# Optimization experiments

Hardware: AMD Instinct MI355X
Metric: run time of the kernel (lower is better)

Reference implementation:

```python
import jax, jax.numpy as jnp
import numpy as np

TOP_K = 4
EPS = 1e-6


def setup_inputs() -> dict:
    key = jax.random.key(0)
    k1, k2, k3 = jax.random.split(key, 3)
    B, Q, N, H, W = 4, 200, 32, 256, 256
    pred_masks = jax.random.normal(k1, (B, Q, H, W), dtype=jnp.float32)
    pred_logits = jax.random.normal(k2, (B, Q, 2), dtype=jnp.float32)
    gt_masks = (jax.random.uniform(k3, (B, N, H, W)) < 0.3).astype(jnp.float32)
    return {"pred_masks": pred_masks, "pred_logits": pred_logits, "gt_masks": gt_masks}


def _combined_scores(pred_masks, pred_logits, gt_masks):
    """IoU * class-score, shape [B, Q, N]."""
    pm = jax.nn.sigmoid(pred_masks)                    # [B,Q,H,W]
    cls = jax.nn.softmax(pred_logits, axis=-1)[..., 1]  # [B,Q]
    B, Q = pm.shape[:2]
    N = gt_masks.shape[1]
    pmf = pm.reshape(B, Q, -1)                         # [B,Q,D]
    tmf = gt_masks.reshape(B, N, -1)                   # [B,N,D]
    inter = jnp.einsum('bqd,bnd->bqn', pmf, tmf)
    union = pmf.sum(-1)[:, :, None] + tmf.sum(-1)[:, None, :] - inter
    iou = inter / (union + EPS)
    return iou * cls[:, :, None]


def _greedy_assign(combined):
    """Greedy per-GT top-k with dedup. combined: [Q,N] -> sel indices [N,k], -1 = dropped."""
    Q = combined.shape[0]
    k = min(TOP_K, Q)

    def step(assigned, col):
        _, idx = jax.lax.top_k(col, k)          # [k] query indices for this GT
        taken = assigned[idx]                   # already assigned -> drop
        sel = jnp.where(taken, -1, idx)
        assigned = assigned.at[idx].set(True)
        return assigned, sel

    _, sels = jax.lax.scan(step, jnp.zeros(Q, dtype=bool), combined.T)
    return sels  # [N, k]


def reference(pred_masks, pred_logits, gt_masks):
    combined = _combined_scores(pred_masks, pred_logits, gt_masks)  # [B,Q,N]
    sels = jax.vmap(_greedy_assign)(combined)                       # [B,N,k]
    B, N, k = sels.shape
    src_idx = sels
    tgt_idx = jnp.broadcast_to(jnp.arange(N, dtype=jnp.int32)[None, :, None], sels.shape)
    valid = sels >= 0
    tgt_idx = jnp.where(valid, tgt_idx, -1)
    return src_idx, tgt_idx, valid
```

## Files before the change

kernel.cpp:

```cpp
#include <hip/hip_runtime.h>
#include <math.h>
#include <stdint.h>

#define BB    4
#define QQ    200
#define NGT   32
#define DD    65536
#define TOPK  4
#define EPSF  1e-6f
#define QP    208

#define QT3   7
#define KS    32
#define KC    (DD / KS)
#define BK    128
#define NCH   (KC / BK)
#define NSTEP (BK / 16)
#define BKP   (BK + 8)

typedef float  f32x4  __attribute__((ext_vector_type(4)));
typedef float  f32x16 __attribute__((ext_vector_type(16)));
typedef __bf16 bf16x8 __attribute__((ext_vector_type(8)));

__global__ __launch_bounds__(256) void k_pack(const float* __restrict__ gt,
                                              uint32_t* __restrict__ packed,
                                              float* __restrict__ zero_base) {
    int zidx = blockIdx.x * 256 + threadIdx.x;
    if (zidx < BB * NGT * QP + BB * QP) zero_base[zidx] = 0.0f;

    int blk = blockIdx.x;
    int b = blk >> 6;
    int d0 = ((blk & 63) * 256 + threadIdx.x) * 4;
    uint32_t px = 0, py = 0, pz = 0, pw = 0;
    const float* gb = gt + (size_t)b * NGT * DD + d0;
#pragma unroll
    for (int n = 0; n < NGT; ++n) {
        float4 g = *(const float4*)(gb + (size_t)n * DD);
        px |= (g.x > 0.5f ? 1u : 0u) << n;
        py |= (g.y > 0.5f ? 1u : 0u) << n;
        pz |= (g.z > 0.5f ? 1u : 0u) << n;
        pw |= (g.w > 0.5f ? 1u : 0u) << n;
    }
    *(uint4*)(packed + (size_t)b * DD + d0) = make_uint4(px, py, pz, pw);
}

__global__ __launch_bounds__(256) void k_tsum(const uint32_t* __restrict__ packed,
                                              float* __restrict__ tsum,
                                              const float* __restrict__ logits,
                                              float* __restrict__ cls) {
    if (blockIdx.x < 4) {
        int i = blockIdx.x * 256 + threadIdx.x;
        if (i < BB * QQ) {
            float l0 = logits[2 * i], l1 = logits[2 * i + 1];
            cls[i] = 1.0f / (1.0f + expf(l0 - l1));
        }
    }
    int b = blockIdx.x >> 5;
    int n = blockIdx.x & 31;
    const uint4* pp = (const uint4*)(packed + (size_t)b * DD);
    int cnt = 0;
    for (int i = threadIdx.x; i < DD / 4; i += 256) {
        uint4 w = pp[i];
        cnt += (int)((w.x >> n) & 1u) + (int)((w.y >> n) & 1u) +
               (int)((w.z >> n) & 1u) + (int)((w.w >> n) & 1u);
    }
#pragma unroll
    for (int off = 32; off; off >>= 1) cnt += __shfl_xor(cnt, off);
    __shared__ int red[4];
    if ((threadIdx.x & 63) == 0) red[threadIdx.x >> 6] = cnt;
    __syncthreads();
    if (threadIdx.x == 0)
        tsum[blockIdx.x] = (float)(red[0] + red[1] + red[2] + red[3]);
}

__global__ __launch_bounds__(256, 3) void k_mfma(const float* __restrict__ pm,
                                                 const uint32_t* __restrict__ packed,
                                                 float* __restrict__ inter,
                                                 float* __restrict__ psum) {
    int blk = blockIdx.x;
    int b   = blk / (QT3 * KS);
    int rem = blk % (QT3 * KS);
    int qt  = rem / KS;
    int ks  = rem % KS;
    int tid = threadIdx.x, lane = tid & 63, wave = tid >> 6;

    __shared__ __bf16 aA[3][32][BKP];
    __shared__ uint32_t bfrag[NSTEP * 256];

    int q_local = tid >> 3;
    int dseg    = (tid & 7) * 16;
    int q_glob  = qt * 32 + q_local;
    int q_eff   = q_glob < QQ ? q_glob : QQ - 1;
    const float*    pmrow = pm + (size_t)(b * QQ + q_eff) * DD + ks * KC;
    const uint32_t* pk    = packed + (size_t)b * DD + ks * KC;

    int l0  = (tid * 2) & 63;
    int bst = tid >> 5;
    int bko = bst * 16 + ((l0 >> 5) << 3);
    int sh0 = 31 - (l0 & 31);
    int sh1 = 31 - ((l0 + 1) & 31);

    int m    = lane & 31;
    int half = lane >> 5;

    f32x16 ch_, cm_, cl_;
#pragma unroll
    for (int r = 0; r < 16; ++r) { ch_[r] = 0.f; cm_[r] = 0.f; cl_[r] = 0.f; }
    float ps = 0.f;

    for (int ch = 0; ch < NCH; ++ch) {
        const float* src = pmrow + ch * BK + dseg;
        float4 f0 = *(const float4*)(src);
        float4 f1 = *(const float4*)(src + 4);
        float4 f2 = *(const float4*)(src + 8);
        float4 f3 = *(const float4*)(src + 12);
        float xv[16] = {f0.x, f0.y, f0.z, f0.w, f1.x, f1.y, f1.z, f1.w,
                        f2.x, f2.y, f2.z, f2.w, f3.x, f3.y, f3.z, f3.w};
        uint32_t hd[8], md[8], ld[8];
#pragma unroll
        for (int p = 0; p < 8; ++p) {
            uint32_t uh[2], um[2], ul[2];
#pragma unroll
            for (int e = 0; e < 2; ++e) {
                float x = xv[2 * p + e];
                float s = __builtin_amdgcn_rcpf(1.0f + __expf(-x));
                ps += s;
                uint32_t u0 = __float_as_uint(s);
                float hi = __uint_as_float(u0 & 0xFFFF0000u);
                float r1 = s - hi;
                uint32_t u1 = __float_as_uint(r1);
                float mi = __uint_as_float(u1 & 0xFFFF0000u);
                float r2 = r1 - mi;
                uh[e] = u0; um[e] = u1; ul[e] = __float_as_uint(r2);
            }
            hd[p] = (uh[0] >> 16) | (uh[1] & 0xFFFF0000u);
            md[p] = (um[0] >> 16) | (um[1] & 0xFFFF0000u);
            ld[p] = (ul[0] >> 16) | (ul[1] & 0xFFFF0000u);
        }
        uint4 wa = *(const uint4*)(pk + ch * BK + bko);
        uint4 wb = *(const uint4*)(pk + ch * BK + bko + 4);
        uint32_t w[8] = {wa.x, wa.y, wa.z, wa.w, wb.x, wb.y, wb.z, wb.w};
        uint32_t bv[8];
#pragma unroll
        for (int dw = 0; dw < 4; ++dw) {
            bv[dw]     = (uint32_t)(((int)(w[2 * dw] << sh0) >> 31) & 0x3F80)
                       | (uint32_t)(((int)(w[2 * dw + 1] << sh0) >> 31) & 0x3F800000);
            bv[4 + dw] = (uint32_t)(((int)(w[2 * dw] << sh1) >> 31) & 0x3F80)
                       | (uint32_t)(((int)(w[2 * dw + 1] << sh1) >> 31) & 0x3F800000);
        }

        __syncthreads();
        *(uint4*)&aA[0][q_local][dseg]     = make_uint4(hd[0], hd[1], hd[2], hd[3]);
        *(uint4*)&aA[0][q_local][dseg + 8] = make_uint4(hd[4], hd[5], hd[6], hd[7]);
        *(uint4*)&aA[1][q_local][dseg]     = make_uint4(md[0], md[1], md[2], md[3]);
        *(uint4*)&aA[1][q_local][dseg + 8] = make_uint4(md[4], md[5], md[6], md[7]);
        *(uint4*)&aA[2][q_local][dseg]     = make_uint4(ld[0], ld[1], ld[2], ld[3]);
        *(uint4*)&aA[2][q_local][dseg + 8] = make_uint4(ld[4], ld[5], ld[6], ld[7]);
        *(uint4*)&bfrag[tid * 8]     = make_uint4(bv[0], bv[1], bv[2], bv[3]);
        *(uint4*)&bfrag[tid * 8 + 4] = make_uint4(bv[4], bv[5], bv[6], bv[7]);
        __syncthreads();

#pragma unroll
        for (int st = 0; st < 2; ++st) {
            int sidx = wave * 2 + st;
            int k0 = sidx * 16 + half * 8;
            bf16x8 ah = *(const bf16x8*)&aA[0][m][k0];
            bf16x8 am = *(const bf16x8*)&aA[1][m][k0];
            bf16x8 al = *(const bf16x8*)&aA[2][m][k0];
            bf16x8 bb = *(const bf16x8*)&bfrag[sidx * 256 + lane * 4];
            ch_ = __builtin_amdgcn_mfma_f32_32x32x16_bf16(ah, bb, ch_, 0, 0, 0);
            cm_ = __builtin_amdgcn_mfma_f32_32x32x16_bf16(am, bb, cm_, 0, 0, 0);
            cl_ = __builtin_amdgcn_mfma_f32_32x32x16_bf16(al, bb, cl_, 0, 0, 0);
        }
    }

    ps += __shfl_xor(ps, 1);
    ps += __shfl_xor(ps, 2);
    ps += __shfl_xor(ps, 4);
    if ((tid & 7) == 0 && q_glob < QQ) atomicAdd(&psum[b * QP + q_glob], ps);

    f32x16 c;
#pragma unroll
    for (int r = 0; r < 16; ++r) c[r] = ch_[r] + cm_[r] + cl_[r];

    __syncthreads();
    float* cred = (float*)aA;
    if (wave > 0) {
        float* dst = cred + ((size_t)(wave - 1) * 64 + lane) * 16;
#pragma unroll
        for (int r = 0; r < 16; r += 4) {
            f32x4 v = {c[r], c[r + 1], c[r + 2], c[r + 3]};
            *(f32x4*)(dst + r) = v;
        }
    }
    __syncthreads();
    if (wave == 0) {
#pragma unroll
        for (int wv = 0; wv < 3; ++wv) {
            const float* sp = cred + ((size_t)wv * 64 + lane) * 16;
#pragma unroll
            for (int r = 0; r < 16; ++r) c[r] += sp[r];
        }
        int n = lane & 31;
#pragma unroll
        for (int r = 0; r < 16; ++r) {
            int qg = qt * 32 + (r & 3) + 8 * (r >> 2) + 4 * half;
            if (qg < QQ) atomicAdd(&inter[(b * NGT + n) * QP + qg], c[r]);
        }
    }
}

__global__ __launch_bounds__(64) void k_topk(const float* __restrict__ inter,
                                             const float* __restrict__ psum,
                                             const float* __restrict__ tsum,
                                             const float* __restrict__ cls,
                                             int* __restrict__ idx4) {
    int bn = blockIdx.x;
    int b  = bn >> 5;
    int lane = threadIdx.x;
    float tsn = tsum[bn];
    float v[4];
#pragma unroll
    for (int s = 0; s < 4; ++s) {
        int q = lane + 64 * s;
        if (q < QQ) {
            float iv = inter[(size_t)bn * QP + q];
            float un = psum[b * QP + q] + tsn - iv;
            v[s] = iv / (un + EPSF) * cls[b * QQ + q];
        } else {
            v[s] = -INFINITY;
        }
    }
    for (int k = 0; k < TOPK; ++k) {
        float bv = -INFINITY;
        int   bi = 0x7fffffff;
#pragma unroll
        for (int s = 0; s < 4; ++s)
            if (v[s] > bv) { bv = v[s]; bi = lane + 64 * s; }
#pragma unroll
        for (int off = 32; off; off >>= 1) {
            float ov = __shfl_xor(bv, off);
            int   oi = __shfl_xor(bi, off);
            if (ov > bv || (ov == bv && oi < bi)) { bv = ov; bi = oi; }
        }
        if (lane == (bi & 63)) v[bi >> 6] = -INFINITY;
        if (lane == 0) idx4[bn * TOPK + k] = bi;
    }
}

__global__ __launch_bounds__(64) void k_final(const int* __restrict__ idx4,
                                              int* __restrict__ out) {
    int b = blockIdx.x;
    int lane = threadIdx.x;
    int* src = out;
    int* tgt = out + BB * NGT * TOPK;
    int* val = out + 2 * BB * NGT * TOPK;
    int asg = 0;
    for (int n = 0; n < NGT; ++n) {
        int4 id = *(const int4*)&idx4[(b * NGT + n) * TOPK];
        int ids[4] = {id.x, id.y, id.z, id.w};
        int newasg = asg;
#pragma unroll
        for (int k = 0; k < TOPK; ++k) {
            int idx = ids[k];
            int owner = idx & 63, slot = idx >> 6;
            int oasg = __shfl(asg, owner);
            int taken = (oasg >> slot) & 1;
            if (lane == owner) newasg |= (1 << slot);
            if (lane == 0) {
                int o = (b * NGT + n) * TOPK + k;
                src[o] = taken ? -1 : idx;
                tgt[o] = taken ? -1 : n;
                val[o] = taken ? 0 : 1;
            }
        }
        asg = newasg;
    }
}

extern "C" void kernel_launch(void* const* d_in, const int* in_sizes, int n_in,
                              void* d_out, int out_size, void* d_ws, size_t ws_size,
                              hipStream_t stream) {
    const float* pred_masks  = (const float*)d_in[0];
    const float* pred_logits = (const float*)d_in[1];
    const float* gt_masks    = (const float*)d_in[2];

    uint8_t* ws = (uint8_t*)d_ws;
    uint32_t* packed = (uint32_t*)ws;
    float* tsum  = (float*)(ws + (size_t)BB * DD * 4);
    float* inter = tsum + BB * NGT;
    float* psum  = inter + BB * NGT * QP;
    float* cls   = psum + BB * QP;
    int*   idx4  = (int*)(cls + BB * QQ);

    k_pack <<<BB * (DD / 1024), 256, 0, stream>>>(gt_masks, packed, inter);
    k_tsum <<<BB * NGT,         256, 0, stream>>>(packed, tsum, pred_logits, cls);
    k_mfma <<<BB * QT3 * KS,    256, 0, stream>>>(pred_masks, packed, inter, psum);
    k_topk <<<BB * NGT,          64, 0, stream>>>(inter, psum, tsum, cls, idx4);
    k_final<<<BB,                64, 0, stream>>>(idx4, (int*)d_out);
}
```

Measured before the change: 369.6 us.

## Load MFMA operands directly into registers, dropping LDS staging and barriers

The mask-intersection kernel no longer stages the bf16-split sigmoid values and the expanded GT bits through shared memory. Each wave now loads its own 256-wide K slice straight into MFMA register fragments, prefetches the next step, and issues the MFMAs with no per-chunk __syncthreads. The grid doubles to 64 K-groups and the kernel targets 4 blocks per CU. The hi/mid/lo split now uses two accumulators instead of three, the cross-wave reduction buffer is padded, and the class softmax moves from k_tsum into k_topk. In exchange, global loads are narrower per lane (32 bytes per row) and there are more atomics from the larger grid.

```diff
diff --git a/kernel.cpp b/kernel.cpp
--- a/kernel.cpp
+++ b/kernel.cpp
@@ -11,12 +11,8 @@
 #define QP    208
 
 #define QT3   7
-#define KS    32
-#define KC    (DD / KS)
-#define BK    128
-#define NCH   (KC / BK)
-#define NSTEP (BK / 16)
-#define BKP   (BK + 8)
+#define KG    64
+#define NSTEP 16
 
 typedef float  f32x4  __attribute__((ext_vector_type(4)));
 typedef float  f32x16 __attribute__((ext_vector_type(16)));
@@ -45,16 +41,7 @@
 }
 
 __global__ __launch_bounds__(256) void k_tsum(const uint32_t* __restrict__ packed,
-                                              float* __restrict__ tsum,
-                                              const float* __restrict__ logits,
-                                              float* __restrict__ cls) {
-    if (blockIdx.x < 4) {
-        int i = blockIdx.x * 256 + threadIdx.x;
-        if (i < BB * QQ) {
-            float l0 = logits[2 * i], l1 = logits[2 * i + 1];
-            cls[i] = 1.0f / (1.0f + expf(l0 - l1));
-        }
-    }
+                                              float* __restrict__ tsum) {
     int b = blockIdx.x >> 5;
     int n = blockIdx.x & 31;
     const uint4* pp = (const uint4*)(packed + (size_t)b * DD);
@@ -73,139 +60,112 @@
         tsum[blockIdx.x] = (float)(red[0] + red[1] + red[2] + red[3]);
 }
 
-__global__ __launch_bounds__(256, 3) void k_mfma(const float* __restrict__ pm,
+__global__ __launch_bounds__(256, 4) void k_mfma(const float* __restrict__ pm,
                                                  const uint32_t* __restrict__ packed,
                                                  float* __restrict__ inter,
                                                  float* __restrict__ psum) {
     int blk = blockIdx.x;
-    int b   = blk / (QT3 * KS);
-    int rem = blk % (QT3 * KS);
-    int qt  = rem / KS;
-    int ks  = rem % KS;
+    int b   = blk / (QT3 * KG);
+    int rem = blk % (QT3 * KG);
+    int qt  = rem / KG;
+    int kg  = rem % KG;
     int tid = threadIdx.x, lane = tid & 63, wave = tid >> 6;
-
-    __shared__ __bf16 aA[3][32][BKP];
-    __shared__ uint32_t bfrag[NSTEP * 256];
-
-    int q_local = tid >> 3;
-    int dseg    = (tid & 7) * 16;
-    int q_glob  = qt * 32 + q_local;
-    int q_eff   = q_glob < QQ ? q_glob : QQ - 1;
-    const float*    pmrow = pm + (size_t)(b * QQ + q_eff) * DD + ks * KC;
-    const uint32_t* pk    = packed + (size_t)b * DD + ks * KC;
-
-    int l0  = (tid * 2) & 63;
-    int bst = tid >> 5;
-    int bko = bst * 16 + ((l0 >> 5) << 3);
-    int sh0 = 31 - (l0 & 31);
-    int sh1 = 31 - ((l0 + 1) & 31);
-
-    int m    = lane & 31;
-    int half = lane >> 5;
-
-    f32x16 ch_, cm_, cl_;
-#pragma unroll
-    for (int r = 0; r < 16; ++r) { ch_[r] = 0.f; cm_[r] = 0.f; cl_[r] = 0.f; }
+    int m = lane & 31, half = lane >> 5;
+
+    int q_glob = qt * 32 + m;
+    int q_eff  = q_glob < QQ ? q_glob : QQ - 1;
+    int kbase  = kg * 1024 + wave * 256;
+    const float*    ap = pm + (size_t)(b * QQ + q_eff) * DD + kbase + half * 8;
+    const uint32_t* bp = packed + (size_t)b * DD + kbase + half * 8;
+
+    f32x16 c0, c1;
+#pragma unroll
+    for (int r = 0; r < 16; ++r) { c0[r] = 0.f; c1[r] = 0.f; }
     float ps = 0.f;
-
-    for (int ch = 0; ch < NCH; ++ch) {
-        const float* src = pmrow + ch * BK + dseg;
-        float4 f0 = *(const float4*)(src);
-        float4 f1 = *(const float4*)(src + 4);
-        float4 f2 = *(const float4*)(src + 8);
-        float4 f3 = *(const float4*)(src + 12);
-        float xv[16] = {f0.x, f0.y, f0.z, f0.w, f1.x, f1.y, f1.z, f1.w,
-                        f2.x, f2.y, f2.z, f2.w, f3.x, f3.y, f3.z, f3.w};
-        uint32_t hd[8], md[8], ld[8];
-#pragma unroll
-        for (int p = 0; p < 8; ++p) {
-            uint32_t uh[2], um[2], ul[2];
-#pragma unroll
-            for (int e = 0; e < 2; ++e) {
-                float x = xv[2 * p + e];
-                float s = __builtin_amdgcn_rcpf(1.0f + __expf(-x));
-                ps += s;
-                uint32_t u0 = __float_as_uint(s);
-                float hi = __uint_as_float(u0 & 0xFFFF0000u);
-                float r1 = s - hi;
-                uint32_t u1 = __float_as_uint(r1);
-                float mi = __uint_as_float(u1 & 0xFFFF0000u);
-                float r2 = r1 - mi;
-                uh[e] = u0; um[e] = u1; ul[e] = __float_as_uint(r2);
-            }
-            hd[p] = (uh[0] >> 16) | (uh[1] & 0xFFFF0000u);
-            md[p] = (um[0] >> 16) | (um[1] & 0xFFFF0000u);
-            ld[p] = (ul[0] >> 16) | (ul[1] & 0xFFFF0000u);
-        }
-        uint4 wa = *(const uint4*)(pk + ch * BK + bko);
-        uint4 wb = *(const uint4*)(pk + ch * BK + bko + 4);
-        uint32_t w[8] = {wa.x, wa.y, wa.z, wa.w, wb.x, wb.y, wb.z, wb.w};
-        uint32_t bv[8];
-#pragma unroll
-        for (int dw = 0; dw < 4; ++dw) {
-            bv[dw]     = (uint32_t)(((int)(w[2 * dw] << sh0) >> 31) & 0x3F80)
-                       | (uint32_t)(((int)(w[2 * dw + 1] << sh0) >> 31) & 0x3F800000);
-            bv[4 + dw] = (uint32_t)(((int)(w[2 * dw] << sh1) >> 31) & 0x3F80)
-                       | (uint32_t)(((int)(w[2 * dw + 1] << sh1) >> 31) & 0x3F800000);
-        }
-
-        __syncthreads();
-        *(uint4*)&aA[0][q_local][dseg]     = make_uint4(hd[0], hd[1], hd[2], hd[3]);
-        *(uint4*)&aA[0][q_local][dseg + 8] = make_uint4(hd[4], hd[5], hd[6], hd[7]);
-        *(uint4*)&aA[1][q_local][dseg]     = make_uint4(md[0], md[1], md[2], md[3]);
-        *(uint4*)&aA[1][q_local][dseg + 8] = make_uint4(md[4], md[5], md[6], md[7]);
-        *(uint4*)&aA[2][q_local][dseg]     = make_uint4(ld[0], ld[1], ld[2], ld[3]);
-        *(uint4*)&aA[2][q_local][dseg + 8] = make_uint4(ld[4], ld[5], ld[6], ld[7]);
-        *(uint4*)&bfrag[tid * 8]     = make_uint4(bv[0], bv[1], bv[2], bv[3]);
-        *(uint4*)&bfrag[tid * 8 + 4] = make_uint4(bv[4], bv[5], bv[6], bv[7]);
-        __syncthreads();
-
-#pragma unroll
-        for (int st = 0; st < 2; ++st) {
-            int sidx = wave * 2 + st;
-            int k0 = sidx * 16 + half * 8;
-            bf16x8 ah = *(const bf16x8*)&aA[0][m][k0];
-            bf16x8 am = *(const bf16x8*)&aA[1][m][k0];
-            bf16x8 al = *(const bf16x8*)&aA[2][m][k0];
-            bf16x8 bb = *(const bf16x8*)&bfrag[sidx * 256 + lane * 4];
-            ch_ = __builtin_amdgcn_mfma_f32_32x32x16_bf16(ah, bb, ch_, 0, 0, 0);
-            cm_ = __builtin_amdgcn_mfma_f32_32x32x16_bf16(am, bb, cm_, 0, 0, 0);
-            cl_ = __builtin_amdgcn_mfma_f32_32x32x16_bf16(al, bb, cl_, 0, 0, 0);
-        }
-    }
-
-    ps += __shfl_xor(ps, 1);
-    ps += __shfl_xor(ps, 2);
-    ps += __shfl_xor(ps, 4);
-    if ((tid & 7) == 0 && q_glob < QQ) atomicAdd(&psum[b * QP + q_glob], ps);
+    int sh = 31 - m;
+
+    float4 fa0 = *(const float4*)ap;
+    float4 fa1 = *(const float4*)(ap + 4);
+    uint4  wb0 = *(const uint4*)bp;
+    uint4  wb1 = *(const uint4*)(bp + 4);
+
+    for (int s = 0; s < NSTEP; ++s) {
+        float4 a0 = fa0, a1 = fa1;
+        uint4  w0 = wb0, w1 = wb1;
+        if (s < NSTEP - 1) {
+            const float*    apn = ap + (s + 1) * 16;
+            const uint32_t* bpn = bp + (s + 1) * 16;
+            fa0 = *(const float4*)apn;
+            fa1 = *(const float4*)(apn + 4);
+            wb0 = *(const uint4*)bpn;
+            wb1 = *(const uint4*)(bpn + 4);
+        }
+        float xs[8] = {a0.x, a0.y, a0.z, a0.w, a1.x, a1.y, a1.z, a1.w};
+        uint32_t hu[8], mu[8], lu[8];
+#pragma unroll
+        for (int i = 0; i < 8; ++i) {
+            float x  = xs[i];
+            float sg = __builtin_amdgcn_rcpf(1.0f + __expf(-x));
+            ps += sg;
+            uint32_t u0 = __float_as_uint(sg);
+            float hi = __uint_as_float(u0 & 0xFFFF0000u);
+            float r1 = sg - hi;
+            uint32_t u1 = __float_as_uint(r1);
+            float mi = __uint_as_float(u1 & 0xFFFF0000u);
+            float r2 = r1 - mi;
+            hu[i] = u0; mu[i] = u1; lu[i] = __float_as_uint(r2);
+        }
+        union { uint4 u; bf16x8 v; } ah, am, al, bb;
+        ah.u = make_uint4((hu[0] >> 16) | (hu[1] & 0xFFFF0000u),
+                          (hu[2] >> 16) | (hu[3] & 0xFFFF0000u),
+                          (hu[4] >> 16) | (hu[5] & 0xFFFF0000u),
+                          (hu[6] >> 16) | (hu[7] & 0xFFFF0000u));
+        am.u = make_uint4((mu[0] >> 16) | (mu[1] & 0xFFFF0000u),
+                          (mu[2] >> 16) | (mu[3] & 0xFFFF0000u),
+                          (mu[4] >> 16) | (mu[5] & 0xFFFF0000u),
+                          (mu[6] >> 16) | (mu[7] & 0xFFFF0000u));
+        al.u = make_uint4((lu[0] >> 16) | (lu[1] & 0xFFFF0000u),
+                          (lu[2] >> 16) | (lu[3] & 0xFFFF0000u),
+                          (lu[4] >> 16) | (lu[5] & 0xFFFF0000u),
+                          (lu[6] >> 16) | (lu[7] & 0xFFFF0000u));
+        uint32_t wj[8] = {w0.x, w0.y, w0.z, w0.w, w1.x, w1.y, w1.z, w1.w};
+        uint32_t bv[4];
+#pragma unroll
+        for (int d = 0; d < 4; ++d)
+            bv[d] = ((uint32_t)(((int)(wj[2 * d] << sh)) >> 31) & 0x3F80u)
+                  | ((uint32_t)(((int)(wj[2 * d + 1] << sh)) >> 31) & 0x3F800000u);
+        bb.u = make_uint4(bv[0], bv[1], bv[2], bv[3]);
+
+        c0 = __builtin_amdgcn_mfma_f32_32x32x16_bf16(ah.v, bb.v, c0, 0, 0, 0);
+        c1 = __builtin_amdgcn_mfma_f32_32x32x16_bf16(am.v, bb.v, c1, 0, 0, 0);
+        c1 = __builtin_amdgcn_mfma_f32_32x32x16_bf16(al.v, bb.v, c1, 0, 0, 0);
+    }
+
+    ps += __shfl_xor(ps, 32);
+    if (lane < 32 && q_glob < QQ) atomicAdd(&psum[b * QP + q_glob], ps);
 
     f32x16 c;
 #pragma unroll
-    for (int r = 0; r < 16; ++r) c[r] = ch_[r] + cm_[r] + cl_[r];
-
-    __syncthreads();
-    float* cred = (float*)aA;
+    for (int r = 0; r < 16; ++r) c[r] = c0[r] + c1[r];
+
+    __shared__ float cred[3 * 64 * 17];
     if (wave > 0) {
-        float* dst = cred + ((size_t)(wave - 1) * 64 + lane) * 16;
-#pragma unroll
-        for (int r = 0; r < 16; r += 4) {
-            f32x4 v = {c[r], c[r + 1], c[r + 2], c[r + 3]};
-            *(f32x4*)(dst + r) = v;
-        }
+        float* dst = cred + ((wave - 1) * 64 + lane) * 17;
+#pragma unroll
+        for (int r = 0; r < 16; ++r) dst[r] = c[r];
     }
     __syncthreads();
     if (wave == 0) {
 #pragma unroll
         for (int wv = 0; wv < 3; ++wv) {
-            const float* sp = cred + ((size_t)wv * 64 + lane) * 16;
+            const float* sp = cred + (wv * 64 + lane) * 17;
 #pragma unroll
             for (int r = 0; r < 16; ++r) c[r] += sp[r];
         }
-        int n = lane & 31;
 #pragma unroll
         for (int r = 0; r < 16; ++r) {
             int qg = qt * 32 + (r & 3) + 8 * (r >> 2) + 4 * half;
-            if (qg < QQ) atomicAdd(&inter[(b * NGT + n) * QP + qg], c[r]);
+            if (qg < QQ) atomicAdd(&inter[(b * NGT + m) * QP + qg], c[r]);
         }
     }
 }
@@ -213,7 +173,7 @@
 __global__ __launch_bounds__(64) void k_topk(const float* __restrict__ inter,
                                              const float* __restrict__ psum,
                                              const float* __restrict__ tsum,
-                                             const float* __restrict__ cls,
+                                             const float* __restrict__ logits,
                                              int* __restrict__ idx4) {
     int bn = blockIdx.x;
     int b  = bn >> 5;
@@ -226,7 +186,10 @@
         if (q < QQ) {
             float iv = inter[(size_t)bn * QP + q];
             float un = psum[b * QP + q] + tsn - iv;
-            v[s] = iv / (un + EPSF) * cls[b * QQ + q];
+            float l0 = logits[(b * QQ + q) * 2];
+            float l1 = logits[(b * QQ + q) * 2 + 1];
+            float cl = 1.0f / (1.0f + expf(l0 - l1));
+            v[s] = iv / (un + EPSF) * cl;
         } else {
             v[s] = -INFINITY;
         }
@@ -290,12 +253,11 @@
     float* tsum  = (float*)(ws + (size_t)BB * DD * 4);
     float* inter = tsum + BB * NGT;
     float* psum  = inter + BB * NGT * QP;
-    float* cls   = psum + BB * QP;
-    int*   idx4  = (int*)(cls + BB * QQ);
+    int*   idx4  = (int*)(psum + BB * QP);
 
     k_pack <<<BB * (DD / 1024), 256, 0, stream>>>(gt_masks, packed, inter);
-    k_tsum <<<BB * NGT,         256, 0, stream>>>(packed, tsum, pred_logits, cls);
-    k_mfma <<<BB * QT3 * KS,    256, 0, stream>>>(pred_masks, packed, inter, psum);
-    k_topk <<<BB * NGT,          64, 0, stream>>>(inter, psum, tsum, cls, idx4);
+    k_tsum <<<BB * NGT,         256, 0, stream>>>(packed, tsum);
+    k_mfma <<<BB * QT3 * KG,    256, 0, stream>>>(pred_masks, packed, inter, psum);
+    k_topk <<<BB * NGT,          64, 0, stream>>>(inter, psum, tsum, pred_logits, idx4);
     k_final<<<BB,                64, 0, stream>>>(idx4, (int*)d_out);
 }
```

Result: slower. 382.9 us (+3.6%).
